# Kernel tuning notes

Measured on AMD Instinct MI355X. Metric: run time of the kernel, lower is better.

Reference implementation:

```python
import jax, jax.numpy as jnp
import numpy as np

N = 100000
H = 20            # horizon
C = 36            # classes
MV = 200000       # vehicle edges
MO = 400000       # obstacle edges
STEP = 2.0        # TRAJECTORY_PIONTS_LENGTH
DIST_COST = 1.0
OBS_COST = 1.0
OBS_RADIUS = 1.0
VEH_COST = 1.0
VEH_RADIUS = 2.0


def setup_inputs() -> dict:
    key = jax.random.key(0)
    k1, k2, k3, k4, k5, k6 = jax.random.split(key, 6)
    # X: [type, x, y, t_x/r, t_y]; all rows vehicles (type 0) so trajectories are live
    feats = jax.random.normal(k1, (N, 4), dtype=jnp.float32) * 10.0
    X = jnp.concatenate([jnp.zeros((N, 1), jnp.float32), feats], axis=1)
    prediction = jax.random.normal(k2, (N, H * C), dtype=jnp.float32)
    ev0 = jax.random.randint(k3, (MV,), 0, N, dtype=jnp.int32)
    off = jax.random.randint(k4, (MV,), 1, N, dtype=jnp.int32)
    ev1 = (ev0 + off) % N  # guarantee no self-edges
    edges_vehicles = jnp.stack([ev0, ev1], axis=0)
    eo0 = jax.random.randint(k5, (MO,), 0, N, dtype=jnp.int32)
    eo1 = jax.random.randint(k6, (MO,), 0, N, dtype=jnp.int32)
    edges_obstacles = jnp.stack([eo0, eo1], axis=0)
    return {"X": X, "prediction": prediction,
            "edges_vehicles": edges_vehicles, "edges_obstacles": edges_obstacles}


def reference(X, prediction, edges_vehicles, edges_obstacles):
    # class decoding: angle = argmax_class * (2pi/C) * max_logit
    pred = prediction.reshape(-1, H, C)
    max_vals = jnp.max(pred, axis=-1)                      # (N,H)
    max_cls = jnp.argmax(pred, axis=-1).astype(pred.dtype)  # (N,H)
    ang = max_cls * (2.0 * np.pi / C) * max_vals
    vec = jnp.stack([jnp.cos(ang), jnp.sin(ang)], axis=-1)  # (N,H,2)

    vmask = X[:, 0] == 0
    # sequential rollout == cumulative sum of unit steps from initial position
    traj = X[:, None, 1:3] + jnp.cumsum(vec * STEP, axis=1)  # (N,H,2)
    traj = jnp.where(vmask[:, None, None], traj, 0.0)

    # distance to target, mean over vehicle rows x horizon
    d = jnp.linalg.norm(X[:, None, 3:5] - traj, axis=-1)    # (N,H)
    nveh = jnp.sum(vmask).astype(d.dtype)
    distance_loss = jnp.sum(jnp.where(vmask[:, None], d, 0.0)) / (nveh * H) * DIST_COST

    # obstacle term: gather obstacle rows and trajectory rows along edges
    fo = X[edges_obstacles[0]]                               # (MO,5)
    tt = traj[edges_obstacles[1]]                            # (MO,H,2)
    od = jnp.linalg.norm(fo[:, None, 1:3] - tt, axis=-1)     # (MO,H)
    onear = od < fo[:, None, 3] + OBS_RADIUS
    osafe = jnp.where(onear, od, 1.0)
    ocnt = jnp.sum(onear)
    osum = jnp.sum(jnp.where(onear, 1.0 / osafe, 0.0))
    obstacle_loss = jnp.where(ocnt > 0, osum / jnp.maximum(ocnt, 1), 0.0) * OBS_COST

    # vehicle term: all-pairs horizon-step distances per edge
    ft = traj[edges_vehicles[0]]                             # (MV,H,2)
    tt2 = traj[edges_vehicles[1]]                            # (MV,H,2)
    vd = jnp.linalg.norm(ft[:, :, None, :] - tt2[:, None, :, :], axis=-1)  # (MV,H,H)
    vnear = vd < VEH_RADIUS
    vsafe = jnp.where(vnear, vd, 1.0)
    vcnt = jnp.sum(vnear)
    vsum = jnp.sum(jnp.where(vnear, 1.0 / vsafe, 0.0))
    vehicle_loss = jnp.where(vcnt > 0, vsum / jnp.maximum(vcnt, 1), 0.0) * VEH_COST

    total = distance_loss + obstacle_loss + vehicle_loss
    return (total, distance_loss, obstacle_loss, vehicle_loss)
```

## Files before the change

kernel.cpp:

```cpp
#include <hip/hip_runtime.h>
#include <math.h>

#define HORIZON 20
#define NCLASS  36
constexpr float STEP = 2.0f;
constexpr float TWO_PI_OVER_C = 0.17453292519943295f;
constexpr float OBS_RADIUS = 1.0f;

template <int BS>
__device__ __forceinline__ void block_commit(float sum, unsigned cnt,
                                             float* __restrict__ pOut,
                                             unsigned* __restrict__ cOut,
                                             int slot) {
    __shared__ float    ls[BS / 64];
    __shared__ unsigned lc[BS / 64];
    #pragma unroll
    for (int off = 32; off > 0; off >>= 1) {
        sum += __shfl_down(sum, off, 64);
        cnt += __shfl_down(cnt, off, 64);
    }
    int wid = threadIdx.x >> 6;
    if ((threadIdx.x & 63) == 0) { ls[wid] = sum; lc[wid] = cnt; }
    __syncthreads();
    if (threadIdx.x == 0) {
        float s = 0.0f; unsigned c = 0u;
        #pragma unroll
        for (int w = 0; w < BS / 64; w++) { s += ls[w]; c += lc[w]; }
        pOut[slot] = s;
        cOut[slot] = c;
    }
}

__global__ void __launch_bounds__(256) angles_kernel(const float* __restrict__ pred,
                                                     float2* __restrict__ steps,
                                                     int total_rows) {
    __shared__ float smM[4][576];
    __shared__ float smI[4][576];
    int wave = threadIdx.x >> 6;
    int lane = threadIdx.x & 63;
    int chunk = blockIdx.x * 4 + wave;
    int row0 = chunk * 64;
    int total_f4 = total_rows * 9;
    const float4* p4 = (const float4*)pred;
    #pragma unroll
    for (int q = 0; q < 9; q++) {
        int gl = q * 64 + lane;
        int g = row0 * 9 + gl;
        float4 v;
        if (g < total_f4) v = p4[g];
        else v = make_float4(-INFINITY, -INFINITY, -INFINITY, -INFINITY);
        int j = gl % 9;
        float m = v.x; int ii = 0;
        if (v.y > m) { m = v.y; ii = 1; }
        if (v.z > m) { m = v.z; ii = 2; }
        if (v.w > m) { m = v.w; ii = 3; }
        smM[wave][gl] = m;
        smI[wave][gl] = (float)(j * 4 + ii);
    }
    __syncthreads();
    int row = row0 + lane;
    if (row < total_rows) {
        float best = -INFINITY; float bidx = 0.0f;
        #pragma unroll
        for (int j = 0; j < 9; j++) {
            float m = smM[wave][lane * 9 + j];
            float id = smI[wave][lane * 9 + j];
            if (m > best) { best = m; bidx = id; }
        }
        float ang = bidx * TWO_PI_OVER_C * best;
        float s, c;
        sincosf(ang, &s, &c);
        steps[row] = make_float2(STEP * c, STEP * s);
    }
}

__global__ void __launch_bounds__(256) rollout_kernel(const float* __restrict__ X,
                                                      const float2* __restrict__ steps,
                                                      float2* __restrict__ traj,
                                                      float4* __restrict__ obsInfo,
                                                      float* __restrict__ distP,
                                                      unsigned* __restrict__ distC,
                                                      int n) {
    int i = blockIdx.x * 256 + threadIdx.x;
    float dsum = 0.0f;
    unsigned vehc = 0;
    if (i < n) {
        const float* xr = X + (size_t)i * 5;
        float typ = xr[0];
        float px = xr[1], py = xr[2];
        float tx = xr[3], ty = xr[4];
        float thr = tx + OBS_RADIUS;
        obsInfo[i] = make_float4(px, py, (thr > 0.0f) ? thr * thr : -1.0f, 0.0f);
        bool veh = (typ == 0.0f);
        const float4* sp = (const float4*)(steps + (size_t)i * HORIZON);
        float4 buf[10];
        #pragma unroll
        for (int q = 0; q < 10; q++) buf[q] = sp[q];
        float* f = (float*)buf;
        #pragma unroll
        for (int h = 0; h < HORIZON; h++) {
            px += f[2 * h]; py += f[2 * h + 1];
            float ox = veh ? px : 0.0f;
            float oy = veh ? py : 0.0f;
            f[2 * h] = ox; f[2 * h + 1] = oy;
            float dx = tx - ox, dy = ty - oy;
            dsum += veh ? sqrtf(fmaf(dy, dy, dx * dx)) : 0.0f;
        }
        float4* tp = (float4*)(traj + (size_t)i * HORIZON);
        #pragma unroll
        for (int q = 0; q < 10; q++) tp[q] = buf[q];
        vehc = veh ? 1u : 0u;
    }
    block_commit<256>(dsum, vehc, distP, distC, blockIdx.x);
}

__global__ void __launch_bounds__(256) edges_kernel(const float4* __restrict__ obsInfo,
                                                    const int* __restrict__ eo, int mo,
                                                    const int* __restrict__ ev, int mv,
                                                    const float2* __restrict__ traj,
                                                    float* __restrict__ obsP,
                                                    unsigned* __restrict__ obsC,
                                                    float* __restrict__ vehP,
                                                    unsigned* __restrict__ vehC,
                                                    int nbO) {
    if ((int)blockIdx.x < nbO) {
        int e = blockIdx.x * 256 + threadIdx.x;
        float osum = 0.0f; unsigned ocnt = 0;
        if (e < mo) {
            int src = eo[e];
            int dst = eo[mo + e];
            float4 info = obsInfo[src];
            if (info.z >= 0.0f) {
                const float4* tp = (const float4*)(traj + (size_t)dst * HORIZON);
                float4 buf[10];
                #pragma unroll
                for (int q = 0; q < 10; q++) buf[q] = tp[q];
                const float* f = (const float*)buf;
                #pragma unroll
                for (int h = 0; h < HORIZON; h++) {
                    float dx = info.x - f[2 * h], dy = info.y - f[2 * h + 1];
                    float d2 = fmaf(dy, dy, dx * dx);
                    bool near = d2 < info.z;
                    ocnt += near ? 1u : 0u;
                    osum += near ? rsqrtf(d2) : 0.0f;
                }
            }
        }
        block_commit<256>(osum, ocnt, obsP, obsC, blockIdx.x);
    } else {
        int t = (blockIdx.x - nbO) * 256 + threadIdx.x;
        int e = t >> 1;
        int half = t & 1;
        float vsum = 0.0f; unsigned vcnt = 0;
        if (e < mv) {
            int a = ev[e];
            int b = ev[mv + e];
            const float4* pb = (const float4*)(traj + (size_t)b * HORIZON);
            float4 tb[10];
            #pragma unroll
            for (int q = 0; q < 10; q++) tb[q] = pb[q];
            const float* fb = (const float*)tb;
            const float4* pa = (const float4*)(traj + (size_t)a * HORIZON + half * 10);
            float4 ta[5];
            #pragma unroll
            for (int q = 0; q < 5; q++) ta[q] = pa[q];
            const float* fa = (const float*)ta;
            #pragma unroll
            for (int i = 0; i < 10; i++) {
                float ax = fa[2 * i], ay = fa[2 * i + 1];
                #pragma unroll
                for (int j = 0; j < HORIZON; j++) {
                    float dx = ax - fb[2 * j];
                    float dy = ay - fb[2 * j + 1];
                    float d2 = fmaf(dy, dy, dx * dx);
                    bool near = d2 < 4.0f;
                    vcnt += near ? 1u : 0u;
                    vsum += near ? rsqrtf(d2) : 0.0f;
                }
            }
        }
        block_commit<256>(vsum, vcnt, vehP, vehC, blockIdx.x - nbO);
    }
}

__global__ void __launch_bounds__(256) finalize_kernel(
        const float* __restrict__ distP, const unsigned* __restrict__ distC, int nbR,
        const float* __restrict__ obsP,  const unsigned* __restrict__ obsC,  int nbO,
        const float* __restrict__ vehP,  const unsigned* __restrict__ vehC,  int nbV,
        float* __restrict__ out) {
    double s0 = 0, s1 = 0, s2 = 0;
    unsigned long long c0 = 0, c1 = 0, c2 = 0;
    for (int i = threadIdx.x; i < nbR; i += 256) { s0 += (double)distP[i]; c0 += distC[i]; }
    for (int i = threadIdx.x; i < nbO; i += 256) { s1 += (double)obsP[i];  c1 += obsC[i]; }
    for (int i = threadIdx.x; i < nbV; i += 256) { s2 += (double)vehP[i];  c2 += vehC[i]; }
    __shared__ double ds[3][4];
    __shared__ unsigned long long dc[3][4];
    double sv[3] = {s0, s1, s2};
    unsigned long long cv[3] = {c0, c1, c2};
    #pragma unroll
    for (int k = 0; k < 3; k++) {
        double v = sv[k]; unsigned long long cc = cv[k];
        #pragma unroll
        for (int off = 32; off > 0; off >>= 1) {
            v += __shfl_down(v, off, 64);
            cc += __shfl_down(cc, off, 64);
        }
        if ((threadIdx.x & 63) == 0) { ds[k][threadIdx.x >> 6] = v; dc[k][threadIdx.x >> 6] = cc; }
    }
    __syncthreads();
    if (threadIdx.x == 0) {
        double S[3]; unsigned long long C[3];
        #pragma unroll
        for (int k = 0; k < 3; k++) {
            S[k] = ds[k][0] + ds[k][1] + ds[k][2] + ds[k][3];
            C[k] = dc[k][0] + dc[k][1] + dc[k][2] + dc[k][3];
        }
        float dist = (C[0] > 0) ? (float)(S[0] / ((double)C[0] * (double)HORIZON)) : 0.0f;
        float obs  = (C[1] > 0) ? (float)(S[1] / (double)C[1]) : 0.0f;
        float veh  = (C[2] > 0) ? (float)(S[2] / (double)C[2]) : 0.0f;
        out[0] = dist + obs + veh;
        out[1] = dist;
        out[2] = obs;
        out[3] = veh;
    }
}

extern "C" void kernel_launch(void* const* d_in, const int* in_sizes, int n_in,
                              void* d_out, int out_size, void* d_ws, size_t ws_size,
                              hipStream_t stream) {
    const float* X    = (const float*)d_in[0];
    const float* pred = (const float*)d_in[1];
    const int*   ev   = (const int*)d_in[2];
    const int*   eo   = (const int*)d_in[3];
    int n_nodes = in_sizes[0] / 5;
    int mv = in_sizes[2] / 2;
    int mo = in_sizes[3] / 2;

    int total_rows = n_nodes * HORIZON;
    int nChunks = (total_rows + 63) / 64;
    int nbA = (nChunks + 3) / 4;
    int nbR = (n_nodes + 255) / 256;
    int nbO = (mo + 255) / 256;
    int nbV = (2 * mv + 255) / 256;

    char* w = (char*)d_ws;
    float2* steps = (float2*)w;
    size_t off = (size_t)total_rows * sizeof(float2);
    off = (off + 255) & ~(size_t)255;
    float2* traj = (float2*)(w + off);
    off += (size_t)total_rows * sizeof(float2);
    off = (off + 255) & ~(size_t)255;
    float4* obsInfo = (float4*)(w + off);   off += (size_t)n_nodes * sizeof(float4);
    off = (off + 255) & ~(size_t)255;
    float*    distP = (float*)(w + off);    off += (size_t)nbR * 4;
    unsigned* distC = (unsigned*)(w + off); off += (size_t)nbR * 4;
    float*    obsP  = (float*)(w + off);    off += (size_t)nbO * 4;
    unsigned* obsC  = (unsigned*)(w + off); off += (size_t)nbO * 4;
    float*    vehP  = (float*)(w + off);    off += (size_t)nbV * 4;
    unsigned* vehC  = (unsigned*)(w + off); off += (size_t)nbV * 4;
    float* out = (float*)d_out;

    hipLaunchKernelGGL(angles_kernel, dim3(nbA), dim3(256), 0, stream,
                       pred, steps, total_rows);
    hipLaunchKernelGGL(rollout_kernel, dim3(nbR), dim3(256), 0, stream,
                       X, steps, traj, obsInfo, distP, distC, n_nodes);
    hipLaunchKernelGGL(edges_kernel, dim3(nbO + nbV), dim3(256), 0, stream,
                       obsInfo, eo, mo, ev, mv, traj, obsP, obsC, vehP, vehC, nbO);
    hipLaunchKernelGGL(finalize_kernel, dim3(1), dim3(256), 0, stream,
                       distP, distC, nbR, obsP, obsC, nbO, vehP, vehC, nbV, out);
}
```

Measured before the change: 452.4 us.

## Fuse angle decoding with rollout and share trajectory halves via lane shuffles

Merges the angle-decoding and rollout kernels into one kernel that keeps per-row steps in shared memory. Each 320-thread block decodes 16 nodes and rolls them out, so the intermediate steps array no longer round-trips through global memory and one launch is removed. In the vehicle-edge path, each lane pair now loads half of trajectory b and swaps the other half with a shuffle, cutting redundant gathers. The cost is a serial rollout by only 16 threads per block plus extra synchronisation, which leaves most lanes idle during that phase.

```diff
diff --git a/kernel.cpp b/kernel.cpp
--- a/kernel.cpp
+++ b/kernel.cpp
@@ -6,6 +6,10 @@
 constexpr float STEP = 2.0f;
 constexpr float TWO_PI_OVER_C = 0.17453292519943295f;
 constexpr float OBS_RADIUS = 1.0f;
+
+#define NODES_PER_BLOCK 16
+#define ROWS_PER_BLOCK  (NODES_PER_BLOCK * HORIZON)
+#define FUSED_BS        320
 
 template <int BS>
 __device__ __forceinline__ void block_commit(float sum, unsigned cnt,
@@ -31,16 +35,26 @@
     }
 }
 
-__global__ void __launch_bounds__(256) angles_kernel(const float* __restrict__ pred,
-                                                     float2* __restrict__ steps,
-                                                     int total_rows) {
-    __shared__ float smM[4][576];
-    __shared__ float smI[4][576];
+__global__ void __launch_bounds__(FUSED_BS) fused_rollout_kernel(
+        const float* __restrict__ X,
+        const float* __restrict__ pred,
+        float2* __restrict__ traj,
+        float4* __restrict__ obsInfo,
+        float* __restrict__ distP,
+        unsigned* __restrict__ distC,
+        int n_nodes) {
+    __shared__ float smM[5][576];
+    __shared__ float smI[5][576];
+    __shared__ __align__(16) float2 smSteps[ROWS_PER_BLOCK];
+    __shared__ __align__(16) float2 smTraj[ROWS_PER_BLOCK];
+
+    int total_rows = n_nodes * HORIZON;
+    int total_f4 = total_rows * 9;
     int wave = threadIdx.x >> 6;
     int lane = threadIdx.x & 63;
-    int chunk = blockIdx.x * 4 + wave;
-    int row0 = chunk * 64;
-    int total_f4 = total_rows * 9;
+    int block_row0 = blockIdx.x * ROWS_PER_BLOCK;
+    int row0 = block_row0 + wave * 64;
+
     const float4* p4 = (const float4*)pred;
     #pragma unroll
     for (int q = 0; q < 9; q++) {
@@ -58,8 +72,8 @@
         smI[wave][gl] = (float)(j * 4 + ii);
     }
     __syncthreads();
-    int row = row0 + lane;
-    if (row < total_rows) {
+
+    {
         float best = -INFINITY; float bidx = 0.0f;
         #pragma unroll
         for (int j = 0; j < 9; j++) {
@@ -70,48 +84,49 @@
         float ang = bidx * TWO_PI_OVER_C * best;
         float s, c;
         sincosf(ang, &s, &c);
-        steps[row] = make_float2(STEP * c, STEP * s);
-    }
-}
-
-__global__ void __launch_bounds__(256) rollout_kernel(const float* __restrict__ X,
-                                                      const float2* __restrict__ steps,
-                                                      float2* __restrict__ traj,
-                                                      float4* __restrict__ obsInfo,
-                                                      float* __restrict__ distP,
-                                                      unsigned* __restrict__ distC,
-                                                      int n) {
-    int i = blockIdx.x * 256 + threadIdx.x;
+        smSteps[threadIdx.x] = make_float2(STEP * c, STEP * s);
+    }
+    __syncthreads();
+
     float dsum = 0.0f;
-    unsigned vehc = 0;
-    if (i < n) {
-        const float* xr = X + (size_t)i * 5;
-        float typ = xr[0];
-        float px = xr[1], py = xr[2];
-        float tx = xr[3], ty = xr[4];
-        float thr = tx + OBS_RADIUS;
-        obsInfo[i] = make_float4(px, py, (thr > 0.0f) ? thr * thr : -1.0f, 0.0f);
-        bool veh = (typ == 0.0f);
-        const float4* sp = (const float4*)(steps + (size_t)i * HORIZON);
-        float4 buf[10];
-        #pragma unroll
-        for (int q = 0; q < 10; q++) buf[q] = sp[q];
-        float* f = (float*)buf;
-        #pragma unroll
-        for (int h = 0; h < HORIZON; h++) {
-            px += f[2 * h]; py += f[2 * h + 1];
-            float ox = veh ? px : 0.0f;
-            float oy = veh ? py : 0.0f;
-            f[2 * h] = ox; f[2 * h + 1] = oy;
-            float dx = tx - ox, dy = ty - oy;
-            dsum += veh ? sqrtf(fmaf(dy, dy, dx * dx)) : 0.0f;
-        }
-        float4* tp = (float4*)(traj + (size_t)i * HORIZON);
-        #pragma unroll
-        for (int q = 0; q < 10; q++) tp[q] = buf[q];
-        vehc = veh ? 1u : 0u;
-    }
-    block_commit<256>(dsum, vehc, distP, distC, blockIdx.x);
+    unsigned vehc = 0u;
+    if (threadIdx.x < NODES_PER_BLOCK) {
+        int g = blockIdx.x * NODES_PER_BLOCK + threadIdx.x;
+        if (g < n_nodes) {
+            const float* xr = X + (size_t)g * 5;
+            float typ = xr[0];
+            float px = xr[1], py = xr[2];
+            float tx = xr[3], ty = xr[4];
+            float thr = tx + OBS_RADIUS;
+            obsInfo[g] = make_float4(px, py, (thr > 0.0f) ? thr * thr : -1.0f, 0.0f);
+            bool veh = (typ == 0.0f);
+            #pragma unroll
+            for (int h = 0; h < HORIZON; h++) {
+                float2 st = smSteps[threadIdx.x * HORIZON + h];
+                px += st.x; py += st.y;
+                float ox = veh ? px : 0.0f;
+                float oy = veh ? py : 0.0f;
+                smTraj[threadIdx.x * HORIZON + h] = make_float2(ox, oy);
+                float dx = tx - ox, dy = ty - oy;
+                dsum += veh ? sqrtf(fmaf(dy, dy, dx * dx)) : 0.0f;
+            }
+            vehc = veh ? 1u : 0u;
+        }
+    }
+    __syncthreads();
+
+    int rows_in_blk = min(ROWS_PER_BLOCK, total_rows - block_row0);
+    if (rows_in_blk == ROWS_PER_BLOCK) {
+        if (threadIdx.x < ROWS_PER_BLOCK / 2) {
+            ((float4*)(traj + block_row0))[threadIdx.x] =
+                ((const float4*)smTraj)[threadIdx.x];
+        }
+    } else {
+        for (int r = threadIdx.x; r < rows_in_blk; r += FUSED_BS)
+            traj[block_row0 + r] = smTraj[r];
+    }
+
+    block_commit<FUSED_BS>(dsum, vehc, distP, distC, blockIdx.x);
 }
 
 __global__ void __launch_bounds__(256) edges_kernel(const float4* __restrict__ obsInfo,
@@ -155,15 +170,19 @@
         if (e < mv) {
             int a = ev[e];
             int b = ev[mv + e];
-            const float4* pb = (const float4*)(traj + (size_t)b * HORIZON);
-            float4 tb[10];
-            #pragma unroll
-            for (int q = 0; q < 10; q++) tb[q] = pb[q];
-            const float* fb = (const float*)tb;
             const float4* pa = (const float4*)(traj + (size_t)a * HORIZON + half * 10);
-            float4 ta[5];
-            #pragma unroll
-            for (int q = 0; q < 5; q++) ta[q] = pa[q];
+            const float4* pb = (const float4*)(traj + (size_t)b * HORIZON + half * 10);
+            float4 ta[5], tbh[5];
+            #pragma unroll
+            for (int q = 0; q < 5; q++) { ta[q] = pa[q]; tbh[q] = pb[q]; }
+            float fb[40];
+            const float* ft = (const float*)tbh;
+            #pragma unroll
+            for (int k = 0; k < 20; k++) {
+                float other = __shfl_xor(ft[k], 1, 64);
+                fb[k]      = (half == 0) ? ft[k] : other;
+                fb[20 + k] = (half == 0) ? other : ft[k];
+            }
             const float* fa = (const float*)ta;
             #pragma unroll
             for (int i = 0; i < 10; i++) {
@@ -237,35 +256,29 @@
     int mo = in_sizes[3] / 2;
 
     int total_rows = n_nodes * HORIZON;
-    int nChunks = (total_rows + 63) / 64;
-    int nbA = (nChunks + 3) / 4;
-    int nbR = (n_nodes + 255) / 256;
+    int nbF = (n_nodes + NODES_PER_BLOCK - 1) / NODES_PER_BLOCK;
     int nbO = (mo + 255) / 256;
     int nbV = (2 * mv + 255) / 256;
 
     char* w = (char*)d_ws;
-    float2* steps = (float2*)w;
-    size_t off = (size_t)total_rows * sizeof(float2);
-    off = (off + 255) & ~(size_t)255;
+    size_t off = 0;
     float2* traj = (float2*)(w + off);
     off += (size_t)total_rows * sizeof(float2);
     off = (off + 255) & ~(size_t)255;
     float4* obsInfo = (float4*)(w + off);   off += (size_t)n_nodes * sizeof(float4);
     off = (off + 255) & ~(size_t)255;
-    float*    distP = (float*)(w + off);    off += (size_t)nbR * 4;
-    unsigned* distC = (unsigned*)(w + off); off += (size_t)nbR * 4;
+    float*    distP = (float*)(w + off);    off += (size_t)nbF * 4;
+    unsigned* distC = (unsigned*)(w + off); off += (size_t)nbF * 4;
     float*    obsP  = (float*)(w + off);    off += (size_t)nbO * 4;
     unsigned* obsC  = (unsigned*)(w + off); off += (size_t)nbO * 4;
     float*    vehP  = (float*)(w + off);    off += (size_t)nbV * 4;
     unsigned* vehC  = (unsigned*)(w + off); off += (size_t)nbV * 4;
     float* out = (float*)d_out;
 
-    hipLaunchKernelGGL(angles_kernel, dim3(nbA), dim3(256), 0, stream,
-                       pred, steps, total_rows);
-    hipLaunchKernelGGL(rollout_kernel, dim3(nbR), dim3(256), 0, stream,
-                       X, steps, traj, obsInfo, distP, distC, n_nodes);
+    hipLaunchKernelGGL(fused_rollout_kernel, dim3(nbF), dim3(FUSED_BS), 0, stream,
+                       X, pred, traj, obsInfo, distP, distC, n_nodes);
     hipLaunchKernelGGL(edges_kernel, dim3(nbO + nbV), dim3(256), 0, stream,
                        obsInfo, eo, mo, ev, mv, traj, obsP, obsC, vehP, vehC, nbO);
     hipLaunchKernelGGL(finalize_kernel, dim3(1), dim3(256), 0, stream,
-                       distP, distC, nbR, obsP, obsC, nbO, vehP, vehC, nbV, out);
-}
+                       distP, distC, nbF, obsP, obsC, nbO, vehP, vehC, nbV, out);
+}
```

Measured after the change: 451.9 us. About the same (-0.1%).
